# Kernel optimization log

Hardware: AMD Instinct MI355X
Metric: run time of the kernel (lower is better)

The kernel has to match this reference:

```python
import jax, jax.numpy as jnp
import numpy as np

DIM = 768
HEADS = 8
DHEAD = 64
DEMB = HEADS * DHEAD  # 512
EPS = 1e-5


def layer_norm(x, g, b):
    mu = jnp.mean(x, axis=-1, keepdims=True)
    var = jnp.var(x, axis=-1, keepdims=True)
    return (x - mu) * jax.lax.rsqrt(var + EPS) * g + b


def setup_inputs() -> dict:
    key = jax.random.key(0)
    ks = jax.random.split(key, 9)
    b, t, n_src, n_ltn = 2, 4, 8192, 64
    inv = 1.0 / np.sqrt(DIM)
    return {
        "src": jax.random.normal(ks[0], (b, t, n_src, DIM), jnp.float32),
        "ltn": jax.random.normal(ks[1], (b, t, n_ltn, DIM), jnp.float32),
        "g_src": jnp.ones((DIM,), jnp.float32),
        "b_src": jnp.zeros((DIM,), jnp.float32),
        "g_ltn": jnp.ones((DIM,), jnp.float32),
        "b_ltn": jnp.zeros((DIM,), jnp.float32),
        # weights stored (in, out) so y = x @ W  (== torch Linear with W.T)
        "Wq": jax.random.normal(ks[2], (DIM, DEMB), jnp.float32) * inv,
        "Wkv": jax.random.normal(ks[3], (DIM, 2 * DEMB), jnp.float32) * inv,
        "Wo": jax.random.normal(ks[4], (DEMB, DIM), jnp.float32) * (1.0 / np.sqrt(DEMB)),
    }


def reference(src, ltn, g_src, b_src, g_ltn, b_ltn, Wq, Wkv, Wo):
    b, t, n_ltn, _ = ltn.shape
    n_src = src.shape[2]
    scale = DHEAD ** -0.5

    src_n = layer_norm(src, g_src, b_src)
    ltn_n = layer_norm(ltn, g_ltn, b_ltn)

    q = ltn_n @ Wq                                  # [b,t,nl,DEMB]
    ctx = jnp.concatenate([src_n, ltn_n], axis=-2)  # [b,t,ns+nl,DIM]
    kv = ctx @ Wkv                                  # [b,t,ns+nl,2*DEMB]
    k, v = jnp.split(kv, 2, axis=-1)

    def to_heads(x):  # b t n (h d) -> b h t n d
        B, T, N, _ = x.shape
        return x.reshape(B, T, N, HEADS, DHEAD).transpose(0, 3, 1, 2, 4)

    q, k, v = to_heads(q), to_heads(k), to_heads(v)

    attn = jnp.einsum('bhtid,bhtjd->bhtij', q, k) * scale
    attn = jax.nn.softmax(attn - jax.lax.stop_gradient(attn.max(axis=-1, keepdims=True)), axis=-1)
    out = jnp.einsum('bhtij,bhtjd->bhtid', attn, v)  # [b,h,t,nl,d]

    out = out.transpose(0, 2, 3, 1, 4).reshape(b, t, n_ltn, DEMB)
    return out @ Wo
```

## Files before the change

### kernel.cpp

```cpp
#include <hip/hip_runtime.h>
#include <hip/hip_bf16.h>
#include <type_traits>


#define N_SRC 8192
#define N_LTN 64
#define N_CTX 8256
#define NBT 8
#define MROWS 66048
#define DIMK 768
#define DEMB 512
#define NSPLIT 16
#define NTILES 65

typedef short short8 __attribute__((ext_vector_type(8)));
typedef float floatx4 __attribute__((ext_vector_type(4)));
typedef __attribute__((address_space(1))) void gvoid;
typedef __attribute__((address_space(3))) void lvoid;

__device__ inline ushort f2bf(float f) {
    union { float f; unsigned u; } v; v.f = f;
    unsigned u = v.u;
    return (ushort)((u + 0x7fffu + ((u >> 16) & 1u)) >> 16);
}

__global__ __launch_bounds__(256) void transpose_all(
        const float* __restrict__ Wkv, const float* __restrict__ Wq,
        const float* __restrict__ Wo, ushort* __restrict__ WkvT,
        ushort* __restrict__ WqT, ushort* __restrict__ WoT) {
    __shared__ ushort tile[64][65];
    int z = blockIdx.z;
    const float* in; ushort* out; int R, C;
    if (z == 0)      { in = Wkv; out = WkvT; R = 768; C = 1024; }
    else if (z == 1) { in = Wq;  out = WqT;  R = 768; C = 512;  }
    else             { in = Wo;  out = WoT;  R = 512; C = 768;  }
    int C0 = blockIdx.x * 64, R0 = blockIdx.y * 64;
    if (C0 >= C || R0 >= R) return;
    int tc = threadIdx.x & 63, tr4 = threadIdx.x >> 6;
#pragma unroll
    for (int j = 0; j < 16; j++) {
        int r = tr4 + j * 4;
        tile[r][tc] = f2bf(in[(size_t)(R0 + r) * C + C0 + tc]);
    }
    __syncthreads();
#pragma unroll
    for (int j = 0; j < 16; j++) {
        int c = tr4 + j * 4;
        out[(size_t)(C0 + c) * R + R0 + tc] = tile[tc][c];
    }
}

__global__ __launch_bounds__(256) void ln_kernel(
        const float* __restrict__ src, const float* __restrict__ ltn,
        const float* __restrict__ gs, const float* __restrict__ bs,
        const float* __restrict__ gl, const float* __restrict__ bl,
        ushort* __restrict__ ctx, ushort* __restrict__ qin) {
    int r = blockIdx.x * 4 + (threadIdx.x >> 6);
    int lane = threadIdx.x & 63;
    int bt = r / N_CTX;
    int i = r - bt * N_CTX;
    const float *x, *g, *b;
    int isl = (i >= N_SRC);
    if (!isl) { x = src + ((size_t)bt * N_SRC + i) * DIMK; g = gs; b = bs; }
    else      { x = ltn + ((size_t)bt * N_LTN + (i - N_SRC)) * DIMK; g = gl; b = bl; }
    float4 v[3]; float s = 0.f, s2 = 0.f;
#pragma unroll
    for (int t = 0; t < 3; t++) {
        float4 xv = *(const float4*)(x + t * 256 + lane * 4);
        v[t] = xv;
        s  += xv.x + xv.y + xv.z + xv.w;
        s2 += xv.x * xv.x + xv.y * xv.y + xv.z * xv.z + xv.w * xv.w;
    }
#pragma unroll
    for (int off = 32; off >= 1; off >>= 1) {
        s  += __shfl_xor(s,  off, 64);
        s2 += __shfl_xor(s2, off, 64);
    }
    float mu  = s * (1.0f / 768.0f);
    float var = s2 * (1.0f / 768.0f) - mu * mu;
    float rs  = rsqrtf(var + 1e-5f);
    ushort* crow = ctx + (size_t)r * DIMK;
    ushort* qrow = isl ? (qin + (size_t)(bt * N_LTN + (i - N_SRC)) * DIMK) : nullptr;
#pragma unroll
    for (int t = 0; t < 3; t++) {
        int idx = t * 256 + lane * 4;
        float4 gv = *(const float4*)(g + idx);
        float4 bv = *(const float4*)(b + idx);
        ushort4 u;
        u.x = f2bf((v[t].x - mu) * rs * gv.x + bv.x);
        u.y = f2bf((v[t].y - mu) * rs * gv.y + bv.y);
        u.z = f2bf((v[t].z - mu) * rs * gv.z + bv.z);
        u.w = f2bf((v[t].w - mu) * rs * gv.w + bv.w);
        *(ushort4*)(crow + idx) = u;
        if (isl) *(ushort4*)(qrow + idx) = u;
    }
}

template <typename CT>
__global__ __launch_bounds__(256) void gemm_bt(
        const ushort* __restrict__ A, const ushort* __restrict__ B,
        CT* __restrict__ C, int M, int N, int K) {
    __shared__ ushort lA[128 * 64];
    __shared__ ushort lB[128 * 64];
    int tid = threadIdx.x;
    int lane = tid & 63, wave = tid >> 6;
    int wm = wave >> 1, wn = wave & 1;
    int bn = blockIdx.x, bm = blockIdx.y;

    floatx4 acc[4][4];
#pragma unroll
    for (int mi = 0; mi < 4; mi++)
#pragma unroll
        for (int ni = 0; ni < 4; ni++) acc[mi][ni] = (floatx4){0.f, 0.f, 0.f, 0.f};

    int srow = lane >> 3;
    int schunk = (lane & 7) ^ srow;
    int quad = lane >> 4, lr = lane & 15;
    const int kiters = K >> 6;

    for (int kt = 0; kt < kiters; kt++) {
#pragma unroll
        for (int c2 = 0; c2 < 4; c2++) {
            int row = c2 * 32 + wave * 8 + srow;
            const ushort* gpA = A + ((size_t)(bm * 128 + row) * K + kt * 64 + schunk * 8);
            ushort* lpA = lA + (c2 * 32 + wave * 8) * 64 + lane * 8;
            __builtin_amdgcn_global_load_lds((gvoid*)gpA, (lvoid*)lpA, 16, 0, 0);
            const ushort* gpB = B + ((size_t)(bn * 128 + row) * K + kt * 64 + schunk * 8);
            ushort* lpB = lB + (c2 * 32 + wave * 8) * 64 + lane * 8;
            __builtin_amdgcn_global_load_lds((gvoid*)gpB, (lvoid*)lpB, 16, 0, 0);
        }
        __syncthreads();
#pragma unroll
        for (int ks = 0; ks < 2; ks++) {
            short8 av[4], bv[4];
            int slot = ((ks * 4 + quad) ^ (lane & 7)) * 8;
#pragma unroll
            for (int mi = 0; mi < 4; mi++)
                av[mi] = *(const short8*)(lA + (wm * 64 + mi * 16 + lr) * 64 + slot);
#pragma unroll
            for (int ni = 0; ni < 4; ni++)
                bv[ni] = *(const short8*)(lB + (wn * 64 + ni * 16 + lr) * 64 + slot);
#pragma unroll
            for (int mi = 0; mi < 4; mi++)
#pragma unroll
                for (int ni = 0; ni < 4; ni++)
                    acc[mi][ni] = __builtin_amdgcn_mfma_f32_16x16x32_bf16(
                        av[mi], bv[ni], acc[mi][ni], 0, 0, 0);
        }
        __syncthreads();
    }
#pragma unroll
    for (int mi = 0; mi < 4; mi++)
#pragma unroll
        for (int ni = 0; ni < 4; ni++)
#pragma unroll
            for (int r = 0; r < 4; r++) {
                int row = bm * 128 + wm * 64 + mi * 16 + quad * 4 + r;
                int col = bn * 128 + wn * 64 + ni * 16 + lr;
                float vv = acc[mi][ni][r];
                if constexpr (std::is_same<CT, ushort>::value)
                    C[(size_t)row * N + col] = f2bf(vv);
                else
                    C[(size_t)row * N + col] = vv;
            }
}

template <typename CT>
__global__ __launch_bounds__(512, 2) void gemm256_bt(
        const ushort* __restrict__ A, const ushort* __restrict__ B,
        CT* __restrict__ C, int M, int N, int K) {
    __shared__ ushort lA[2][256 * 64];
    __shared__ ushort lB[2][256 * 64];

    int tid = threadIdx.x;
    int lane = tid & 63, w = tid >> 6;
    int wm = w >> 2, wn = w & 3;
    int quad = lane >> 4, lr = lane & 15;

    int ntile = N >> 8;
    int nwg = gridDim.x;
    int lin = blockIdx.x;
    int swz = (lin & 7) * (nwg >> 3) + (lin >> 3);
    int bn = swz % ntile, bm = swz / ntile;

    const int kiters = K >> 6;

    int srow = lane >> 3;
    int schunk = (lane & 7) ^ srow;
    const ushort* aG = A + (size_t)(bm * 256 + w * 8 + srow) * K + schunk * 8;
    const ushort* bG = B + (size_t)(bn * 256 + w * 8 + srow) * K + schunk * 8;

    auto stageA = [&](int nb, int h, int ktv) {
#pragma unroll
        for (int i = 0; i < 2; i++)
            __builtin_amdgcn_global_load_lds(
                (gvoid*)(aG + (size_t)(h * 128 + i * 64) * K + ktv * 64),
                (lvoid*)(&lA[nb][(h * 128 + i * 64 + w * 8) * 64 + lane * 8]),
                16, 0, 0);
    };
    auto stageB = [&](int nb, int h, int ktv) {
#pragma unroll
        for (int i = 0; i < 2; i++)
            __builtin_amdgcn_global_load_lds(
                (gvoid*)(bG + (size_t)(h * 128 + i * 64) * K + ktv * 64),
                (lvoid*)(&lB[nb][(h * 128 + i * 64 + w * 8) * 64 + lane * 8]),
                16, 0, 0);
    };

    floatx4 acc[8][4];
#pragma unroll
    for (int m = 0; m < 8; m++)
#pragma unroll
        for (int n = 0; n < 4; n++) acc[m][n] = (floatx4){0.f, 0.f, 0.f, 0.f};

    const int arb = (wm * 128 + lr) * 64;
    const int brb = (wn * 64 + lr) * 64;
    const int sl0 = (quad ^ (lr & 7)) * 8;
    const int sl1 = ((4 + quad) ^ (lr & 7)) * 8;

    short8 af[4][2], bf[2][2];

#define G256_FENCE asm volatile("" ::: "memory")
#define G256_BAR do { G256_FENCE; __builtin_amdgcn_s_barrier(); G256_FENCE; } while (0)
#define G256_DSA(mh_) do { _Pragma("unroll") \
    for (int m2 = 0; m2 < 4; m2++) { \
        af[m2][0] = *(const short8*)(lac + arb + ((mh_) * 64 + m2 * 16) * 64 + sl0); \
        af[m2][1] = *(const short8*)(lac + arb + ((mh_) * 64 + m2 * 16) * 64 + sl1); } } while (0)
#define G256_DSB(nh_) do { _Pragma("unroll") \
    for (int n2 = 0; n2 < 2; n2++) { \
        bf[n2][0] = *(const short8*)(lbc + brb + ((nh_) * 32 + n2 * 16) * 64 + sl0); \
        bf[n2][1] = *(const short8*)(lbc + brb + ((nh_) * 32 + n2 * 16) * 64 + sl1); } } while (0)
#define G256_MFMA(mh_, nh_) do { \
    asm volatile("s_waitcnt lgkmcnt(0)"); \
    __builtin_amdgcn_s_setprio(1); \
    _Pragma("unroll") for (int kk = 0; kk < 2; kk++) \
    _Pragma("unroll") for (int m2 = 0; m2 < 4; m2++) \
    _Pragma("unroll") for (int n2 = 0; n2 < 2; n2++) \
        acc[(mh_) * 4 + m2][(nh_) * 2 + n2] = __builtin_amdgcn_mfma_f32_16x16x32_bf16( \
            af[m2][kk], bf[n2][kk], acc[(mh_) * 4 + m2][(nh_) * 2 + n2], 0, 0, 0); \
    __builtin_amdgcn_s_setprio(0); } while (0)

    stageA(0, 0, 0); stageA(0, 1, 0); stageB(0, 0, 0); stageB(0, 1, 0);

    for (int kt = 0; kt < kiters; kt++) {
        int c = kt & 1, nb = c ^ 1;
        int ktn = (kt + 1 < kiters) ? kt + 1 : kt;
        const ushort* lac = lA[c];
        const ushort* lbc = lB[c];

        stageA(nb, 0, ktn);
        asm volatile("s_waitcnt vmcnt(2)" ::: "memory");
        G256_BAR;
        G256_DSA(0); G256_DSB(0);
        G256_MFMA(0, 0);
        G256_BAR;
        G256_DSB(1);
        stageA(nb, 1, ktn);
        G256_BAR;
        G256_MFMA(0, 1);
        G256_BAR;
        G256_DSA(1); G256_DSB(0);
        stageB(nb, 0, ktn);
        G256_BAR;
        G256_MFMA(1, 0);
        G256_BAR;
        G256_DSB(1);
        stageB(nb, 1, ktn);
        G256_BAR;
        G256_MFMA(1, 1);
        G256_BAR;
    }
    asm volatile("s_waitcnt vmcnt(0)" ::: "memory");

#undef G256_FENCE
#undef G256_BAR
#undef G256_DSA
#undef G256_DSB
#undef G256_MFMA

    const int crb = bm * 256 + wm * 128 + quad * 4;
    const int ccb = bn * 256 + wn * 64 + lr;
#pragma unroll
    for (int m = 0; m < 8; m++)
#pragma unroll
        for (int n = 0; n < 4; n++)
#pragma unroll
            for (int r = 0; r < 4; r++) {
                int row = crb + m * 16 + r;
                float vv = acc[m][n][r];
                if constexpr (std::is_same<CT, ushort>::value)
                    C[(size_t)row * N + ccb + n * 16] = f2bf(vv);
                else
                    C[(size_t)row * N + ccb + n * 16] = vv;
            }
}

#define PR 136

__global__ __launch_bounds__(256) void attn_flash(
        const float* __restrict__ qf, const ushort* __restrict__ kvb,
        float* __restrict__ Op, float* __restrict__ ml) {
    __shared__ ushort lK[128 * 64];
    __shared__ ushort lVT[64 * PR];
    __shared__ ushort lP[64 * PR];

    int comb = blockIdx.x, split = blockIdx.y;
    int bt = comb >> 3, h = comb & 7;
    int tid = threadIdx.x;
    int w = tid >> 6, lane = tid & 63, quad = lane >> 4, lr = lane & 15;

    const ushort* kptr = kvb + (size_t)bt * N_CTX * 1024 + h * 64;
    const ushort* vptr = kptr + 512;

    short8 qa[2];
    {
        const float* p0 = qf + (size_t)(bt * 64 + w * 16 + lr) * DEMB + h * 64;
#pragma unroll
        for (int kc = 0; kc < 2; kc++) {
            const float* p = p0 + kc * 32 + quad * 8;
            float4 f0 = *(const float4*)p;
            float4 f1 = *(const float4*)(p + 4);
            short8 v;
            v[0] = f2bf(f0.x); v[1] = f2bf(f0.y); v[2] = f2bf(f0.z); v[3] = f2bf(f0.w);
            v[4] = f2bf(f1.x); v[5] = f2bf(f1.y); v[6] = f2bf(f1.z); v[7] = f2bf(f1.w);
            qa[kc] = v;
        }
    }

    floatx4 accO[4];
#pragma unroll
    for (int nt = 0; nt < 4; nt++) accO[nt] = (floatx4){0.f, 0.f, 0.f, 0.f};
    float m_run[4], l_run[4];
#pragma unroll
    for (int r = 0; r < 4; r++) { m_run[r] = -1e30f; l_run[r] = 0.f; }

    for (int t = split; t < NTILES; t += NSPLIT) {
        int kbase = t * 128;
        __syncthreads();

#pragma unroll
        for (int c2 = 0; c2 < 4; c2++) {
            int jloc = w * 32 + c2 * 8 + (lane >> 3);
            int chunk = (lane & 7) ^ ((lane >> 3) & 7);
            int jg = kbase + jloc; if (jg > N_CTX - 1) jg = N_CTX - 1;
            const ushort* gp = kptr + (size_t)jg * 1024 + chunk * 8;
            ushort* lp = lK + (w * 32 + c2 * 8) * 64 + lane * 8;
            __builtin_amdgcn_global_load_lds((gvoid*)gp, (lvoid*)lp, 16, 0, 0);
        }

        {
            int k0 = kbase + lane * 2;
            bool valid = (k0 + 1) < N_CTX;
            int k0c = valid ? k0 : (N_CTX - 2);
            const ushort* r0 = vptr + (size_t)k0c * 1024 + w * 16;
            const ushort* r1 = r0 + 1024;
            uint4 a0 = *(const uint4*)r0;
            uint4 a1 = *(const uint4*)(r0 + 8);
            uint4 b0 = *(const uint4*)r1;
            uint4 b1 = *(const uint4*)(r1 + 8);
            if (!valid) {
                a0 = make_uint4(0, 0, 0, 0); a1 = a0; b0 = a0; b1 = a0;
            }
            unsigned av8[8] = {a0.x, a0.y, a0.z, a0.w, a1.x, a1.y, a1.z, a1.w};
            unsigned bv8[8] = {b0.x, b0.y, b0.z, b0.w, b1.x, b1.y, b1.z, b1.w};
#pragma unroll
            for (int i = 0; i < 8; i++) {
                unsigned la = av8[i] & 0xffffu, ha = av8[i] >> 16;
                unsigned lb = bv8[i] & 0xffffu, hb = bv8[i] >> 16;
                *(unsigned*)(lVT + (w * 16 + 2 * i) * PR + lane * 2)     = la | (lb << 16);
                *(unsigned*)(lVT + (w * 16 + 2 * i + 1) * PR + lane * 2) = ha | (hb << 16);
            }
        }
        __syncthreads();

        floatx4 accS[8];
#pragma unroll
        for (int nt = 0; nt < 8; nt++) accS[nt] = (floatx4){0.f, 0.f, 0.f, 0.f};
#pragma unroll
        for (int kc = 0; kc < 2; kc++) {
#pragma unroll
            for (int nt = 0; nt < 8; nt++) {
                int kr = nt * 16 + lr;
                int slot = (kc * 4 + quad) ^ (kr & 7);
                short8 bv = *(const short8*)(lK + kr * 64 + slot * 8);
                accS[nt] = __builtin_amdgcn_mfma_f32_16x16x32_bf16(
                    qa[kc], bv, accS[nt], 0, 0, 0);
            }
        }

        float sc[8][4];
        float tmax[4] = {-1e30f, -1e30f, -1e30f, -1e30f};
#pragma unroll
        for (int nt = 0; nt < 8; nt++) {
            bool vk = (kbase + nt * 16 + lr) < N_CTX;
#pragma unroll
            for (int r = 0; r < 4; r++) {
                float s = vk ? accS[nt][r] * 0.125f : -1e30f;
                sc[nt][r] = s;
                tmax[r] = fmaxf(tmax[r], s);
            }
        }
#pragma unroll
        for (int r = 0; r < 4; r++) {
#pragma unroll
            for (int d = 1; d < 16; d <<= 1) tmax[r] = fmaxf(tmax[r], __shfl_xor(tmax[r], d, 64));
        }
        float alpha[4], lsum[4];
#pragma unroll
        for (int r = 0; r < 4; r++) {
            float mn = fmaxf(m_run[r], tmax[r]);
            alpha[r] = __expf(m_run[r] - mn);
            m_run[r] = mn;
            lsum[r] = 0.f;
        }

#pragma unroll
        for (int nt = 0; nt < 8; nt++) {
#pragma unroll
            for (int r = 0; r < 4; r++) {
                float p = __expf(sc[nt][r] - m_run[r]);
                lsum[r] += p;
                lP[(w * 16 + quad * 4 + r) * PR + nt * 16 + lr] = f2bf(p);
            }
        }
#pragma unroll
        for (int r = 0; r < 4; r++) {
#pragma unroll
            for (int d = 1; d < 16; d <<= 1) lsum[r] += __shfl_xor(lsum[r], d, 64);
            l_run[r] = l_run[r] * alpha[r] + lsum[r];
        }
#pragma unroll
        for (int nt = 0; nt < 4; nt++) {
            accO[nt][0] *= alpha[0]; accO[nt][1] *= alpha[1];
            accO[nt][2] *= alpha[2]; accO[nt][3] *= alpha[3];
        }

        short8 av[4];
#pragma unroll
        for (int kc = 0; kc < 4; kc++)
            av[kc] = *(const short8*)(lP + (w * 16 + lr) * PR + kc * 32 + quad * 8);
#pragma unroll
        for (int nt = 0; nt < 4; nt++)
#pragma unroll
            for (int kc = 0; kc < 4; kc++) {
                short8 bv = *(const short8*)(lVT + (nt * 16 + lr) * PR + kc * 32 + quad * 8);
                accO[nt] = __builtin_amdgcn_mfma_f32_16x16x32_bf16(av[kc], bv, accO[nt], 0, 0, 0);
            }
    }

    float* opb = Op + (size_t)(comb * NSPLIT + split) * 64 * 64;
#pragma unroll
    for (int nt = 0; nt < 4; nt++)
#pragma unroll
        for (int r = 0; r < 4; r++)
            opb[(w * 16 + quad * 4 + r) * 64 + nt * 16 + lr] = accO[nt][r];
    if (lr == 0) {
#pragma unroll
        for (int r = 0; r < 4; r++) {
            int row = w * 16 + quad * 4 + r;
            float* mlp = ml + ((size_t)(comb * NSPLIT + split) * 64 + row) * 2;
            mlp[0] = m_run[r]; mlp[1] = l_run[r];
        }
    }
}

__global__ __launch_bounds__(64) void attn_combine(
        const float* __restrict__ Op, const float* __restrict__ ml,
        ushort* __restrict__ outp) {
    int bx = blockIdx.x;
    int comb = bx >> 6, q = bx & 63;
    int bt = comb >> 3, h = comb & 7;
    int d = threadIdx.x;
    float M = -1e30f;
    for (int s = 0; s < NSPLIT; s++)
        M = fmaxf(M, ml[((size_t)(comb * NSPLIT + s) * 64 + q) * 2]);
    float L = 0.f, O = 0.f;
    for (int s = 0; s < NSPLIT; s++) {
        const float* p = ml + ((size_t)(comb * NSPLIT + s) * 64 + q) * 2;
        float wgt = __expf(p[0] - M);
        L = fmaf(wgt, p[1], L);
        O = fmaf(wgt, Op[((size_t)(comb * NSPLIT + s) * 64 + q) * 64 + d], O);
    }
    outp[(size_t)(bt * 64 + q) * DEMB + h * 64 + d] = f2bf(O / L);
}

extern "C" void kernel_launch(void* const* d_in, const int* in_sizes, int n_in,
                              void* d_out, int out_size, void* d_ws, size_t ws_size,
                              hipStream_t stream) {
    const float* src   = (const float*)d_in[0];
    const float* ltn   = (const float*)d_in[1];
    const float* g_src = (const float*)d_in[2];
    const float* b_src = (const float*)d_in[3];
    const float* g_ltn = (const float*)d_in[4];
    const float* b_ltn = (const float*)d_in[5];
    const float* Wq    = (const float*)d_in[6];
    const float* Wkv   = (const float*)d_in[7];
    const float* Wo    = (const float*)d_in[8];
    float* out = (float*)d_out;

    char* ws = (char*)d_ws;
    size_t off = 0;
    auto alloc = [&](size_t bytes) -> void* {
        void* p = ws + off;
        off += (bytes + 255) & ~(size_t)255;
        return p;
    };
    ushort* ctx  = (ushort*)alloc((size_t)MROWS * DIMK * 2);
    ushort* qin  = (ushort*)alloc((size_t)512 * DIMK * 2);
    ushort* WkvT = (ushort*)alloc((size_t)1024 * DIMK * 2);
    ushort* WqT  = (ushort*)alloc((size_t)512 * DIMK * 2);
    ushort* WoT  = (ushort*)alloc((size_t)768 * DEMB * 2);
    ushort* kvb  = (ushort*)alloc((size_t)MROWS * 1024 * 2);
    float*  qf   = (float*) alloc((size_t)512 * DEMB * 4);
    ushort* outp = (ushort*)alloc((size_t)512 * DEMB * 2);

    float* Op  = (float*)(void*)ctx;
    float* mlb = Op + (size_t)64 * NSPLIT * 64 * 64;

    transpose_all<<<dim3(16, 12, 3), 256, 0, stream>>>(Wkv, Wq, Wo, WkvT, WqT, WoT);

    ln_kernel<<<MROWS / 4, 256, 0, stream>>>(src, ltn, g_src, b_src, g_ltn, b_ltn, ctx, qin);

    gemm256_bt<ushort><<<dim3((MROWS / 256) * (1024 / 256)), 512, 0, stream>>>(
        ctx, WkvT, kvb, MROWS, 1024, DIMK);
    gemm_bt<float><<<dim3(512 / 128, 512 / 128), 256, 0, stream>>>(
        qin, WqT, qf, 512, 512, DIMK);

    attn_flash<<<dim3(64, NSPLIT), 256, 0, stream>>>(qf, kvb, Op, mlb);
    attn_combine<<<4096, 64, 0, stream>>>(Op, mlb, outp);

    gemm_bt<float><<<dim3(768 / 128, 512 / 128), 256, 0, stream>>>(
        outp, WoT, out, 512, 768, DEMB);
}
```

Before: 555.6 us.

## Restructure GEMM main loop: issue all prefetches upfront, single barrier phase

```diff
diff --git a/kernel.cpp b/kernel.cpp
--- a/kernel.cpp
+++ b/kernel.cpp
@@ -218,27 +218,8 @@
     const int sl0 = (quad ^ (lr & 7)) * 8;
     const int sl1 = ((4 + quad) ^ (lr & 7)) * 8;
 
-    short8 af[4][2], bf[2][2];
-
 #define G256_FENCE asm volatile("" ::: "memory")
 #define G256_BAR do { G256_FENCE; __builtin_amdgcn_s_barrier(); G256_FENCE; } while (0)
-#define G256_DSA(mh_) do { _Pragma("unroll") \
-    for (int m2 = 0; m2 < 4; m2++) { \
-        af[m2][0] = *(const short8*)(lac + arb + ((mh_) * 64 + m2 * 16) * 64 + sl0); \
-        af[m2][1] = *(const short8*)(lac + arb + ((mh_) * 64 + m2 * 16) * 64 + sl1); } } while (0)
-#define G256_DSB(nh_) do { _Pragma("unroll") \
-    for (int n2 = 0; n2 < 2; n2++) { \
-        bf[n2][0] = *(const short8*)(lbc + brb + ((nh_) * 32 + n2 * 16) * 64 + sl0); \
-        bf[n2][1] = *(const short8*)(lbc + brb + ((nh_) * 32 + n2 * 16) * 64 + sl1); } } while (0)
-#define G256_MFMA(mh_, nh_) do { \
-    asm volatile("s_waitcnt lgkmcnt(0)"); \
-    __builtin_amdgcn_s_setprio(1); \
-    _Pragma("unroll") for (int kk = 0; kk < 2; kk++) \
-    _Pragma("unroll") for (int m2 = 0; m2 < 4; m2++) \
-    _Pragma("unroll") for (int n2 = 0; n2 < 2; n2++) \
-        acc[(mh_) * 4 + m2][(nh_) * 2 + n2] = __builtin_amdgcn_mfma_f32_16x16x32_bf16( \
-            af[m2][kk], bf[n2][kk], acc[(mh_) * 4 + m2][(nh_) * 2 + n2], 0, 0, 0); \
-    __builtin_amdgcn_s_setprio(0); } while (0)
 
     stageA(0, 0, 0); stageA(0, 1, 0); stageB(0, 0, 0); stageB(0, 1, 0);
 
@@ -248,35 +229,71 @@
         const ushort* lac = lA[c];
         const ushort* lbc = lB[c];
 
-        stageA(nb, 0, ktn);
-        asm volatile("s_waitcnt vmcnt(2)" ::: "memory");
+        stageA(nb, 0, ktn); stageA(nb, 1, ktn);
+        stageB(nb, 0, ktn); stageB(nb, 1, ktn);
+        asm volatile("s_waitcnt vmcnt(8)" ::: "memory");
         G256_BAR;
-        G256_DSA(0); G256_DSB(0);
-        G256_MFMA(0, 0);
-        G256_BAR;
-        G256_DSB(1);
-        stageA(nb, 1, ktn);
-        G256_BAR;
-        G256_MFMA(0, 1);
-        G256_BAR;
-        G256_DSA(1); G256_DSB(0);
-        stageB(nb, 0, ktn);
-        G256_BAR;
-        G256_MFMA(1, 0);
-        G256_BAR;
-        G256_DSB(1);
-        stageB(nb, 1, ktn);
-        G256_BAR;
-        G256_MFMA(1, 1);
+
+        short8 a0[4][2], a1[4][2], b0[2][2], b1[2][2];
+#pragma unroll
+        for (int m2 = 0; m2 < 4; m2++) {
+            a0[m2][0] = *(const short8*)(lac + arb + (m2 * 16) * 64 + sl0);
+            a0[m2][1] = *(const short8*)(lac + arb + (m2 * 16) * 64 + sl1);
+        }
+#pragma unroll
+        for (int n2 = 0; n2 < 2; n2++) {
+            b0[n2][0] = *(const short8*)(lbc + brb + (n2 * 16) * 64 + sl0);
+            b0[n2][1] = *(const short8*)(lbc + brb + (n2 * 16) * 64 + sl1);
+            b1[n2][0] = *(const short8*)(lbc + brb + ((32 + n2 * 16)) * 64 + sl0);
+            b1[n2][1] = *(const short8*)(lbc + brb + ((32 + n2 * 16)) * 64 + sl1);
+        }
+#pragma unroll
+        for (int m2 = 0; m2 < 4; m2++) {
+            a1[m2][0] = *(const short8*)(lac + arb + ((64 + m2 * 16)) * 64 + sl0);
+            a1[m2][1] = *(const short8*)(lac + arb + ((64 + m2 * 16)) * 64 + sl1);
+        }
+
+        __builtin_amdgcn_s_setprio(1);
+#pragma unroll
+        for (int kk = 0; kk < 2; kk++)
+#pragma unroll
+            for (int m2 = 0; m2 < 4; m2++)
+#pragma unroll
+                for (int n2 = 0; n2 < 2; n2++)
+                    acc[m2][n2] = __builtin_amdgcn_mfma_f32_16x16x32_bf16(
+                        a0[m2][kk], b0[n2][kk], acc[m2][n2], 0, 0, 0);
+#pragma unroll
+        for (int kk = 0; kk < 2; kk++)
+#pragma unroll
+            for (int m2 = 0; m2 < 4; m2++)
+#pragma unroll
+                for (int n2 = 0; n2 < 2; n2++)
+                    acc[m2][2 + n2] = __builtin_amdgcn_mfma_f32_16x16x32_bf16(
+                        a0[m2][kk], b1[n2][kk], acc[m2][2 + n2], 0, 0, 0);
+#pragma unroll
+        for (int kk = 0; kk < 2; kk++)
+#pragma unroll
+            for (int m2 = 0; m2 < 4; m2++)
+#pragma unroll
+                for (int n2 = 0; n2 < 2; n2++)
+                    acc[4 + m2][n2] = __builtin_amdgcn_mfma_f32_16x16x32_bf16(
+                        a1[m2][kk], b0[n2][kk], acc[4 + m2][n2], 0, 0, 0);
+#pragma unroll
+        for (int kk = 0; kk < 2; kk++)
+#pragma unroll
+            for (int m2 = 0; m2 < 4; m2++)
+#pragma unroll
+                for (int n2 = 0; n2 < 2; n2++)
+                    acc[4 + m2][2 + n2] = __builtin_amdgcn_mfma_f32_16x16x32_bf16(
+                        a1[m2][kk], b1[n2][kk], acc[4 + m2][2 + n2], 0, 0, 0);
+        __builtin_amdgcn_s_setprio(0);
+
         G256_BAR;
     }
     asm volatile("s_waitcnt vmcnt(0)" ::: "memory");
 
 #undef G256_FENCE
 #undef G256_BAR
-#undef G256_DSA
-#undef G256_DSB
-#undef G256_MFMA
 
     const int crb = bm * 256 + wm * 128 + quad * 4;
     const int ccb = bn * 256 + wn * 64 + lr;
```

After: 539.5 us. -2.9%, faster.
